# Kernel optimization log

Hardware: AMD Instinct MI355X
Metric: run time of the kernel (lower is better)

## Reference

```python
import jax, jax.numpy as jnp
import numpy as np

DIM = 1024
HEADS = 16
DIM_HEAD = 64
INNER = HEADS * DIM_HEAD
SCALE = DIM_HEAD ** -0.5


def rotate_half(t):
    # '... (j d) -> ... j d' with j=2: split last dim in half
    x1, x2 = jnp.split(t, 2, axis=-1)
    return jnp.concatenate((-x2, x1), axis=-1)


def rotary_pos(n, d, dtype):
    inv_freq = 1.0 / (10000.0 ** (jnp.arange(0, d, 2, dtype=jnp.float32) / d))
    freqs = jnp.arange(n, dtype=jnp.float32)[:, None] * inv_freq[None, :]  # (n, d/2)
    return jnp.concatenate((freqs, freqs), axis=-1).astype(dtype)  # (n, d)


def apply_rope(pos, t):
    return t * jnp.cos(pos) + rotate_half(t) * jnp.sin(pos)


def setup_inputs() -> dict:
    key = jax.random.key(0)
    ks = jax.random.split(key, 5)
    x = jax.random.normal(ks[0], (2, 2048, DIM), dtype=jnp.float32)
    gamma = jnp.ones((DIM,), dtype=jnp.float32)
    beta = jnp.zeros((DIM,), dtype=jnp.float32)
    Wq = jax.random.normal(ks[1], (DIM, INNER), dtype=jnp.float32) * 0.02
    Wkv = jax.random.normal(ks[2], (DIM, 2 * INNER), dtype=jnp.float32) * 0.02
    Wo = jax.random.normal(ks[3], (INNER, DIM), dtype=jnp.float32) * 0.02
    return {"x": x, "gamma": gamma, "beta": beta, "Wq": Wq, "Wkv": Wkv, "Wo": Wo}


def reference(x, gamma, beta, Wq, Wkv, Wo):
    b, n, _ = x.shape
    # LayerNorm with learned gamma, fixed-zero beta buffer
    mu = jnp.mean(x, axis=-1, keepdims=True)
    var = jnp.var(x, axis=-1, keepdims=True)
    xn = (x - mu) / jnp.sqrt(var + 1e-5) * gamma + beta

    q = xn @ Wq                       # (b, n, inner)
    kv = xn @ Wkv
    k, v = jnp.split(kv, 2, axis=-1)

    def to_heads(t):
        return t.reshape(b, n, HEADS, DIM_HEAD).transpose(0, 2, 1, 3)  # b h n d

    q, k, v = map(to_heads, (q, k, v))

    pos = rotary_pos(n, DIM_HEAD, x.dtype)  # (n, d)
    q = apply_rope(pos, q)
    k = apply_rope(pos, k)

    q = q * SCALE
    sim = jnp.einsum('bhid,bhjd->bhij', q, k)

    neg = -jnp.finfo(sim.dtype).max
    causal_mask = jnp.triu(jnp.ones((n, n), dtype=bool), k=1)
    sim = jnp.where(causal_mask, neg, sim)

    attn = jax.nn.softmax(sim, axis=-1)
    out = jnp.einsum('bhij,bhjd->bhid', attn, v)
    out = out.transpose(0, 2, 1, 3).reshape(b, n, INNER)
    return out @ Wo
```

## Files before the change

### kernel.cpp

```cpp
#include <hip/hip_runtime.h>
#include <stdint.h>

typedef unsigned short u16;
typedef __attribute__((ext_vector_type(8))) short short8;
typedef __attribute__((ext_vector_type(4))) float floatx4;
typedef __attribute__((ext_vector_type(4))) unsigned short u16x4;
typedef __attribute__((ext_vector_type(2))) unsigned int uint2v;

__device__ __forceinline__ float bf2f(u16 v) {
  union { uint32_t u; float f; } x; x.u = ((uint32_t)v) << 16; return x.f;
}
__device__ __forceinline__ u16 f2bf(float f) {
  union { float f; uint32_t u; } x; x.f = f;
  uint32_t r = x.u + 0x7fffu + ((x.u >> 16) & 1u);
  return (u16)(r >> 16);
}
__device__ __forceinline__ uint32_t fu(float f) {
  union { float f; uint32_t u; } x; x.f = f; return x.u;
}

#define GL2LDS(g, l)                                                          \
  __builtin_amdgcn_global_load_lds(                                           \
      (const __attribute__((address_space(1))) void*)(g),                     \
      (__attribute__((address_space(3))) void*)(l), 16, 0, 0)

__global__ __launch_bounds__(256) void prep_k(const float* __restrict__ x,
                                              const float* __restrict__ gamma,
                                              const float* __restrict__ beta,
                                              const float* __restrict__ Wq,
                                              const float* __restrict__ Wkv,
                                              const float* __restrict__ Wo,
                                              u16* __restrict__ xn,
                                              u16* __restrict__ wqkvT,
                                              u16* __restrict__ woT) {
  int bid = blockIdx.x;
  int t = threadIdx.x;
  if (bid < 4096) {
    int row = bid;
    const float* xr = x + (size_t)row * 1024;
    float4 xv = *(const float4*)(xr + t * 4);
    float v0 = xv.x, v1 = xv.y, v2 = xv.z, v3 = xv.w;
    float s = v0 + v1 + v2 + v3;
    float s2 = v0 * v0 + v1 * v1 + v2 * v2 + v3 * v3;
#pragma unroll
    for (int d = 1; d < 64; d <<= 1) {
      s += __shfl_xor(s, d, 64);
      s2 += __shfl_xor(s2, d, 64);
    }
    __shared__ float red[8];
    int lane = t & 63, wv = t >> 6;
    if (lane == 0) { red[wv] = s; red[4 + wv] = s2; }
    __syncthreads();
    s = red[0] + red[1] + red[2] + red[3];
    s2 = red[4] + red[5] + red[6] + red[7];
    float mu = s * (1.0f / 1024.0f);
    float var = s2 * (1.0f / 1024.0f) - mu * mu;
    float rstd = rsqrtf(var + 1e-5f);
    float4 gv = *(const float4*)(gamma + t * 4);
    float4 bv = *(const float4*)(beta + t * 4);
    u16x4 ov;
    ov.x = f2bf((v0 - mu) * rstd * gv.x + bv.x);
    ov.y = f2bf((v1 - mu) * rstd * gv.y + bv.y);
    ov.z = f2bf((v2 - mu) * rstd * gv.z + bv.z);
    ov.w = f2bf((v3 - mu) * rstd * gv.w + bv.w);
    *(u16x4*)(xn + (size_t)row * 1024 + t * 4) = ov;
  } else {
    __shared__ float tile[32][33];
    int wb = bid - 4096;
    const float* in;
    u16* outp;
    int C;
    if (wb < 1024) { in = Wq; outp = wqkvT; C = 1024; }
    else if (wb < 3072) { wb -= 1024; in = Wkv; outp = wqkvT + 1024 * 1024; C = 2048; }
    else { wb -= 3072; in = Wo; outp = woT; C = 1024; }
    int nbx = C >> 5;
    int c0 = (wb % nbx) * 32, r0 = (wb / nbx) * 32;
    int tx = t & 31, ty = t >> 5;
#pragma unroll
    for (int i = 0; i < 32; i += 8)
      tile[ty + i][tx] = in[(size_t)(r0 + ty + i) * C + c0 + tx];
    __syncthreads();
#pragma unroll
    for (int i = 0; i < 32; i += 8)
      outp[(size_t)(c0 + ty + i) * 1024 + r0 + tx] = f2bf(tile[tx][ty + i]);
  }
}

__global__ __launch_bounds__(256) void gemm_qkv_k(const u16* __restrict__ A,
                                                  const u16* __restrict__ BT,
                                                  u16* __restrict__ C) {
  const int K = 1024, lda = 1024, ldc = 3072;
  __shared__ __align__(16) u16 lA[128 * 32];
  __shared__ __align__(16) u16 lB[128 * 32];
  int tid = threadIdx.x;
  int bm = blockIdx.y * 128;
  int bn = blockIdx.x * 128;
  int w = tid >> 6, l = tid & 63;
  int wm = (w >> 1) * 64, wn = (w & 1) * 64;
  int lr = l & 15, lq = l >> 4;
  floatx4 acc[4][4] = {};
  int sr = w * 16 + (l >> 2);
  int sc = (l & 3) * 8;
  for (int k0 = 0; k0 < K; k0 += 32) {
    GL2LDS(A + (size_t)(bm + sr) * lda + k0 + sc, &lA[sr * 32 + sc]);
    GL2LDS(A + (size_t)(bm + sr + 64) * lda + k0 + sc, &lA[(sr + 64) * 32 + sc]);
    GL2LDS(BT + (size_t)(bn + sr) * K + k0 + sc, &lB[sr * 32 + sc]);
    GL2LDS(BT + (size_t)(bn + sr + 64) * K + k0 + sc, &lB[(sr + 64) * 32 + sc]);
    __syncthreads();
    short8 afr[4], bfr[4];
#pragma unroll
    for (int i = 0; i < 4; i++)
      afr[i] = *(const short8*)(&lA[(wm + i * 16 + lr) * 32 + lq * 8]);
#pragma unroll
    for (int i = 0; i < 4; i++)
      bfr[i] = *(const short8*)(&lB[(wn + i * 16 + lr) * 32 + lq * 8]);
#pragma unroll
    for (int mi = 0; mi < 4; mi++)
#pragma unroll
      for (int ni = 0; ni < 4; ni++)
        acc[mi][ni] = __builtin_amdgcn_mfma_f32_16x16x32_bf16(
            afr[mi], bfr[ni], acc[mi][ni], 0, 0, 0);
    __syncthreads();
  }
  int sec = bn >> 10;
  if (sec == 2) {
#pragma unroll
    for (int mi = 0; mi < 4; mi++)
#pragma unroll
      for (int ni = 0; ni < 4; ni++)
#pragma unroll
        for (int r = 0; r < 4; r++) {
          int row = bm + wm + mi * 16 + lq * 4 + r;
          int col = bn + wn + ni * 16 + lr;
          C[(size_t)row * ldc + col] = f2bf(acc[mi][ni][r]);
        }
  } else {
    float QS = (sec == 0) ? 0.125f * 1.44269504088896f : 1.0f;
#pragma unroll
    for (int ni = 0; ni < 2; ni++) {
      int i = ni * 16 + lr;
      float invf = exp2f(-(float)i * 0.4152410118609203f);
#pragma unroll
      for (int mi = 0; mi < 4; mi++)
#pragma unroll
        for (int r = 0; r < 4; r++) {
          int row = bm + wm + mi * 16 + lq * 4 + r;
          int n = row & 2047;
          float ang = (float)n * invf;
          float s_, c_;
          __sincosf(ang, &s_, &c_);
          float x1 = acc[mi][ni][r], x2 = acc[mi][ni + 2][r];
          int col = bn + wn + ni * 16 + lr;
          C[(size_t)row * ldc + col] = f2bf((x1 * c_ - x2 * s_) * QS);
          C[(size_t)row * ldc + col + 32] = f2bf((x2 * c_ + x1 * s_) * QS);
        }
    }
  }
}

__global__ __launch_bounds__(256) void gemm64_bf16_k(const u16* __restrict__ A,
                                                     const u16* __restrict__ BT,
                                                     float* __restrict__ C,
                                                     int K, int lda, int ldc) {
  __shared__ __align__(16) u16 lA[64 * 32];
  __shared__ __align__(16) u16 lB[128 * 32];
  int tid = threadIdx.x;
  int bm = blockIdx.y * 64;
  int bn = blockIdx.x * 128;
  int w = tid >> 6, l = tid & 63;
  int wm = (w >> 1) * 32, wn = (w & 1) * 64;
  int lr = l & 15, lq = l >> 4;
  floatx4 acc[2][4] = {};
  int sr = w * 16 + (l >> 2);
  int sc = (l & 3) * 8;
  for (int k0 = 0; k0 < K; k0 += 32) {
    GL2LDS(A + (size_t)(bm + sr) * lda + k0 + sc, &lA[sr * 32 + sc]);
    GL2LDS(BT + (size_t)(bn + sr) * K + k0 + sc, &lB[sr * 32 + sc]);
    GL2LDS(BT + (size_t)(bn + sr + 64) * K + k0 + sc, &lB[(sr + 64) * 32 + sc]);
    __syncthreads();
    short8 afr[2], bfr[4];
#pragma unroll
    for (int i = 0; i < 2; i++)
      afr[i] = *(const short8*)(&lA[(wm + i * 16 + lr) * 32 + lq * 8]);
#pragma unroll
    for (int i = 0; i < 4; i++)
      bfr[i] = *(const short8*)(&lB[(wn + i * 16 + lr) * 32 + lq * 8]);
#pragma unroll
    for (int mi = 0; mi < 2; mi++)
#pragma unroll
      for (int ni = 0; ni < 4; ni++)
        acc[mi][ni] = __builtin_amdgcn_mfma_f32_16x16x32_bf16(
            afr[mi], bfr[ni], acc[mi][ni], 0, 0, 0);
    __syncthreads();
  }
#pragma unroll
  for (int mi = 0; mi < 2; mi++)
#pragma unroll
    for (int ni = 0; ni < 4; ni++)
#pragma unroll
      for (int r = 0; r < 4; r++) {
        int row = bm + wm + mi * 16 + lq * 4 + r;
        int col = bn + wn + ni * 16 + lr;
        C[(size_t)row * ldc + col] = acc[mi][ni][r];
      }
}

__global__ __launch_bounds__(256) void vt_k(const u16* __restrict__ qkv,
                                            u16* __restrict__ vT) {
  __shared__ u16 tile[32][33];
  int vb = blockIdx.x;
  int bh = vb >> 7;
  int rest = vb & 127;
  int d0 = (rest >> 6) * 32;
  int n0 = (rest & 63) * 32;
  int b = bh >> 4, h = bh & 15;
  int tid = threadIdx.x;
  int tx = tid & 31, ty = tid >> 5;
#pragma unroll
  for (int i = 0; i < 32; i += 8)
    tile[ty + i][tx] =
        qkv[(size_t)(b * 2048 + n0 + ty + i) * 3072 + 2048 + h * 64 + d0 + tx];
  __syncthreads();
#pragma unroll
  for (int i = 0; i < 32; i += 8)
    vT[((size_t)bh * 64 + d0 + ty + i) * 2048 + n0 + tx] = tile[tx][ty + i];
}

#define LPT 72
#define FIXM 4.0f
__device__ __forceinline__ void attn_tile2(const u16* lK, const u16* lV, u16* lp,
                                           const short8* aq, floatx4* o,
                                           float& l_i, int lr, int lq,
                                           bool diag, int q0, int k0g,
                                           short8 ones) {
  floatx4 s[4];
#pragma unroll
  for (int ni = 0; ni < 4; ni++) {
    floatx4 a = {};
#pragma unroll
    for (int kc = 0; kc < 2; kc++) {
      int R = ni * 16 + lr;
      int c8 = (kc * 4 + lq) ^ (R & 7);
      short8 kf = *(const short8*)&lK[R * 64 + c8 * 8];
      a = __builtin_amdgcn_mfma_f32_16x16x32_bf16(kf, aq[kc], a, 0, 0, 0);
    }
    s[ni] = a;
  }
  if (diag) {
    int qg = q0 + lr;
#pragma unroll
    for (int ni = 0; ni < 4; ni++)
#pragma unroll
      for (int r = 0; r < 4; r++) {
        int kg = k0g + ni * 16 + lq * 4 + r;
        if (kg > qg) s[ni][r] = -1e30f;
      }
  }
#pragma unroll
  for (int ni = 0; ni < 4; ni++) {
    float p0 = exp2f(s[ni][0] - FIXM), p1 = exp2f(s[ni][1] - FIXM);
    float p2 = exp2f(s[ni][2] - FIXM), p3 = exp2f(s[ni][3] - FIXM);
    uint2v dw;
    dw.x = __builtin_amdgcn_perm(fu(p1), fu(p0), 0x07060302u);
    dw.y = __builtin_amdgcn_perm(fu(p3), fu(p2), 0x07060302u);
    *(uint2v*)&lp[lr * LPT + ni * 16 + lq * 4] = dw;
  }
  short8 pb0 = *(const short8*)&lp[lr * LPT + lq * 8];
  short8 pb1 = *(const short8*)&lp[lr * LPT + 32 + lq * 8];
  floatx4 z = {};
  z = __builtin_amdgcn_mfma_f32_16x16x32_bf16(ones, pb0, z, 0, 0, 0);
  z = __builtin_amdgcn_mfma_f32_16x16x32_bf16(ones, pb1, z, 0, 0, 0);
  l_i += z[0];
#pragma unroll
  for (int di = 0; di < 4; di++) {
    int R = di * 16 + lr;
    int c80 = lq ^ (R & 7);
    int c81 = (4 + lq) ^ (R & 7);
    short8 v0 = *(const short8*)&lV[R * 64 + c80 * 8];
    o[di] = __builtin_amdgcn_mfma_f32_16x16x32_bf16(v0, pb0, o[di], 0, 0, 0);
    short8 v1 = *(const short8*)&lV[R * 64 + c81 * 8];
    o[di] = __builtin_amdgcn_mfma_f32_16x16x32_bf16(v1, pb1, o[di], 0, 0, 0);
  }
}

__global__ __launch_bounds__(256) void attn_k(const u16* __restrict__ qkv,
                                              const u16* __restrict__ vt,
                                              u16* __restrict__ out) {
  __shared__ __align__(16) u16 lK[2][64 * 64];
  __shared__ __align__(16) u16 lV[2][64 * 64];
  __shared__ __align__(16) u16 lP[4][16 * LPT];
  int bh = blockIdx.y;
  int b = bh >> 4, h = bh & 15;
  int p = blockIdx.x;
  int jB = 31 - p;
  int tid = threadIdx.x;
  int w = tid >> 6, l = tid & 63;
  int lr = l & 15, lq = l >> 4;
  int q0A = p * 64 + w * 16;
  int q0B = jB * 64 + w * 16;
  const u16* qb = qkv + (size_t)b * 2048 * 3072 + h * 64;
  const u16* kb = qkv + (size_t)b * 2048 * 3072 + 1024 + h * 64;
  const u16* vb = vt + (size_t)bh * 64 * 2048;
  short8 aqA[2], aqB[2];
  aqA[0] = *(const short8*)(qb + (size_t)(q0A + lr) * 3072 + lq * 8);
  aqA[1] = *(const short8*)(qb + (size_t)(q0A + lr) * 3072 + 32 + lq * 8);
  aqB[0] = *(const short8*)(qb + (size_t)(q0B + lr) * 3072 + lq * 8);
  aqB[1] = *(const short8*)(qb + (size_t)(q0B + lr) * 3072 + 32 + lq * 8);
  short8 ones;
#pragma unroll
  for (int i = 0; i < 8; i++) ones[i] = (short)0x3F80;
  floatx4 oA[4] = {}, oB[4] = {};
  float lA_ = 0.0f, lB_ = 0.0f;
  int srow8 = l >> 3;
  int sc8 = (l & 7) ^ srow8;
  u16* lp = &lP[w][0];
  auto stage = [&](int bufi, int kt) {
#pragma unroll
    for (int c = 0; c < 2; c++) {
      int m = w + c * 4;
      int row = m * 8 + srow8;
      GL2LDS(kb + (size_t)(kt * 64 + row) * 3072 + sc8 * 8, &lK[bufi][m * 512]);
      GL2LDS(vb + (size_t)row * 2048 + kt * 64 + sc8 * 8, &lV[bufi][m * 512]);
    }
  };
  stage(0, 0);
  for (int kt = 0; kt <= jB; ++kt) {
    int cur = kt & 1;
    __syncthreads();
    if (kt < jB) stage(cur ^ 1, kt + 1);
    attn_tile2(lK[cur], lV[cur], lp, aqB, oB, lB_, lr, lq, kt == jB, q0B,
               kt * 64, ones);
    if (kt <= p)
      attn_tile2(lK[cur], lV[cur], lp, aqA, oA, lA_, lr, lq, kt == p, q0A,
                 kt * 64, ones);
  }
  float rlA = 1.0f / lA_, rlB = 1.0f / lB_;
#pragma unroll
  for (int di = 0; di < 4; di++) {
    uint2v dwA, dwB;
    u16 a0 = f2bf(oA[di][0] * rlA), a1 = f2bf(oA[di][1] * rlA);
    u16 a2 = f2bf(oA[di][2] * rlA), a3 = f2bf(oA[di][3] * rlA);
    dwA.x = (uint32_t)a0 | ((uint32_t)a1 << 16);
    dwA.y = (uint32_t)a2 | ((uint32_t)a3 << 16);
    u16 b0 = f2bf(oB[di][0] * rlB), b1 = f2bf(oB[di][1] * rlB);
    u16 b2 = f2bf(oB[di][2] * rlB), b3 = f2bf(oB[di][3] * rlB);
    dwB.x = (uint32_t)b0 | ((uint32_t)b1 << 16);
    dwB.y = (uint32_t)b2 | ((uint32_t)b3 << 16);
    int dcol = h * 64 + di * 16 + lq * 4;
    *(uint2v*)(out + ((size_t)(b * 2048 + q0A + lr)) * 3072 + dcol) = dwA;
    *(uint2v*)(out + ((size_t)(b * 2048 + q0B + lr)) * 3072 + dcol) = dwB;
  }
}

extern "C" void kernel_launch(void* const* d_in, const int* in_sizes, int n_in,
                              void* d_out, int out_size, void* d_ws, size_t ws_size,
                              hipStream_t stream) {
  const float* x = (const float*)d_in[0];
  const float* gamma = (const float*)d_in[1];
  const float* beta = (const float*)d_in[2];
  const float* Wq = (const float*)d_in[3];
  const float* Wkv = (const float*)d_in[4];
  const float* Wo = (const float*)d_in[5];
  float* out = (float*)d_out;
  char* ws = (char*)d_ws;

  u16* qkv = (u16*)(ws);
  u16* wqkvT = (u16*)(ws + 25165824);
  u16* woT = (u16*)(ws + 31457280);
  u16* xn = (u16*)(ws + 33554432);
  u16* vT = xn;
  u16* attn_out = qkv + 2048;

  prep_k<<<8192, 256, 0, stream>>>(x, gamma, beta, Wq, Wkv, Wo, xn, wqkvT, woT);
  gemm_qkv_k<<<dim3(24, 32), 256, 0, stream>>>(xn, wqkvT, qkv);
  vt_k<<<4096, 256, 0, stream>>>(qkv, vT);
  attn_k<<<dim3(16, 32), 256, 0, stream>>>(qkv, vT, attn_out);
  gemm64_bf16_k<<<dim3(8, 64), 256, 0, stream>>>(attn_out, woT, out, 1024, 3072, 1024);
}
```

Baseline: 208.9 us.

## Fuse V transpose into QKV GEMM epilogue and simplify attention block scheduling

The QKV GEMM epilogue now writes V already transposed (per batch-head, d-major) into the V section of the qkv buffer, which removes the separate vt_k transpose kernel and its extra global round trip. The attention kernel drops the paired-tile load balancing (pairing q-block p with 31-p) and launches one block per query tile, with batch-head on grid x. Attention output goes to a compact 1024-wide buffer. The per-warp P scratch drops its row padding and uses an XOR swizzle to avoid LDS bank conflicts. Risks are causal work imbalance across blocks and strided 8-byte transposed stores in the GEMM epilogue.

Result: faster. 202.6 us (-3.0%).

```diff
diff --git a/kernel.cpp b/kernel.cpp
--- a/kernel.cpp
+++ b/kernel.cpp
@@ -127,13 +127,22 @@
 #pragma unroll
     for (int mi = 0; mi < 4; mi++)
 #pragma unroll
-      for (int ni = 0; ni < 4; ni++)
-#pragma unroll
-        for (int r = 0; r < 4; r++) {
-          int row = bm + wm + mi * 16 + lq * 4 + r;
-          int col = bn + wn + ni * 16 + lr;
-          C[(size_t)row * ldc + col] = f2bf(acc[mi][ni][r]);
-        }
+      for (int ni = 0; ni < 4; ni++) {
+        int col = bn + wn + ni * 16 + lr;
+        int cv = col - 2048;
+        int row = bm + wm + mi * 16 + lq * 4;
+        int bq = row >> 11;
+        int n = row & 2047;
+        int bh = (bq << 4) | (cv >> 6);
+        int d = cv & 63;
+        size_t L = ((size_t)(bh * 64 + d) << 11) + n;
+        u16x4 ov;
+        ov.x = f2bf(acc[mi][ni][0]);
+        ov.y = f2bf(acc[mi][ni][1]);
+        ov.z = f2bf(acc[mi][ni][2]);
+        ov.w = f2bf(acc[mi][ni][3]);
+        *(u16x4*)(C + (L >> 10) * 3072 + 2048 + (L & 1023)) = ov;
+      }
   } else {
     float QS = (sec == 0) ? 0.125f * 1.44269504088896f : 1.0f;
 #pragma unroll
@@ -205,28 +214,7 @@
       }
 }
 
-__global__ __launch_bounds__(256) void vt_k(const u16* __restrict__ qkv,
-                                            u16* __restrict__ vT) {
-  __shared__ u16 tile[32][33];
-  int vb = blockIdx.x;
-  int bh = vb >> 7;
-  int rest = vb & 127;
-  int d0 = (rest >> 6) * 32;
-  int n0 = (rest & 63) * 32;
-  int b = bh >> 4, h = bh & 15;
-  int tid = threadIdx.x;
-  int tx = tid & 31, ty = tid >> 5;
-#pragma unroll
-  for (int i = 0; i < 32; i += 8)
-    tile[ty + i][tx] =
-        qkv[(size_t)(b * 2048 + n0 + ty + i) * 3072 + 2048 + h * 64 + d0 + tx];
-  __syncthreads();
-#pragma unroll
-  for (int i = 0; i < 32; i += 8)
-    vT[((size_t)bh * 64 + d0 + ty + i) * 2048 + n0 + tx] = tile[tx][ty + i];
-}
-
-#define LPT 72
+#define LPT 64
 #define FIXM 4.0f
 __device__ __forceinline__ void attn_tile2(const u16* lK, const u16* lV, u16* lp,
                                            const short8* aq, floatx4* o,
@@ -256,6 +244,7 @@
         if (kg > qg) s[ni][r] = -1e30f;
       }
   }
+  int swz = (lr & 7) << 3;
 #pragma unroll
   for (int ni = 0; ni < 4; ni++) {
     float p0 = exp2f(s[ni][0] - FIXM), p1 = exp2f(s[ni][1] - FIXM);
@@ -263,10 +252,10 @@
     uint2v dw;
     dw.x = __builtin_amdgcn_perm(fu(p1), fu(p0), 0x07060302u);
     dw.y = __builtin_amdgcn_perm(fu(p3), fu(p2), 0x07060302u);
-    *(uint2v*)&lp[lr * LPT + ni * 16 + lq * 4] = dw;
-  }
-  short8 pb0 = *(const short8*)&lp[lr * LPT + lq * 8];
-  short8 pb1 = *(const short8*)&lp[lr * LPT + 32 + lq * 8];
+    *(uint2v*)&lp[lr * LPT + ((ni * 16 + lq * 4) ^ swz)] = dw;
+  }
+  short8 pb0 = *(const short8*)&lp[lr * LPT + ((lq * 8) ^ swz)];
+  short8 pb1 = *(const short8*)&lp[lr * LPT + ((32 + lq * 8) ^ swz)];
   floatx4 z = {};
   z = __builtin_amdgcn_mfma_f32_16x16x32_bf16(ones, pb0, z, 0, 0, 0);
   z = __builtin_amdgcn_mfma_f32_16x16x32_bf16(ones, pb1, z, 0, 0, 0);
@@ -284,33 +273,28 @@
 }
 
 __global__ __launch_bounds__(256) void attn_k(const u16* __restrict__ qkv,
-                                              const u16* __restrict__ vt,
                                               u16* __restrict__ out) {
   __shared__ __align__(16) u16 lK[2][64 * 64];
   __shared__ __align__(16) u16 lV[2][64 * 64];
   __shared__ __align__(16) u16 lP[4][16 * LPT];
-  int bh = blockIdx.y;
+  int bh = blockIdx.x;
   int b = bh >> 4, h = bh & 15;
-  int p = blockIdx.x;
-  int jB = 31 - p;
+  int j = blockIdx.y;
   int tid = threadIdx.x;
   int w = tid >> 6, l = tid & 63;
   int lr = l & 15, lq = l >> 4;
-  int q0A = p * 64 + w * 16;
-  int q0B = jB * 64 + w * 16;
+  int q0 = j * 64 + w * 16;
   const u16* qb = qkv + (size_t)b * 2048 * 3072 + h * 64;
   const u16* kb = qkv + (size_t)b * 2048 * 3072 + 1024 + h * 64;
-  const u16* vb = vt + (size_t)bh * 64 * 2048;
-  short8 aqA[2], aqB[2];
-  aqA[0] = *(const short8*)(qb + (size_t)(q0A + lr) * 3072 + lq * 8);
-  aqA[1] = *(const short8*)(qb + (size_t)(q0A + lr) * 3072 + 32 + lq * 8);
-  aqB[0] = *(const short8*)(qb + (size_t)(q0B + lr) * 3072 + lq * 8);
-  aqB[1] = *(const short8*)(qb + (size_t)(q0B + lr) * 3072 + 32 + lq * 8);
+  int bh64 = bh * 64;
+  short8 aq[2];
+  aq[0] = *(const short8*)(qb + (size_t)(q0 + lr) * 3072 + lq * 8);
+  aq[1] = *(const short8*)(qb + (size_t)(q0 + lr) * 3072 + 32 + lq * 8);
   short8 ones;
 #pragma unroll
   for (int i = 0; i < 8; i++) ones[i] = (short)0x3F80;
-  floatx4 oA[4] = {}, oB[4] = {};
-  float lA_ = 0.0f, lB_ = 0.0f;
+  floatx4 o[4] = {};
+  float l_ = 0.0f;
   int srow8 = l >> 3;
   int sc8 = (l & 7) ^ srow8;
   u16* lp = &lP[w][0];
@@ -320,35 +304,30 @@
       int m = w + c * 4;
       int row = m * 8 + srow8;
       GL2LDS(kb + (size_t)(kt * 64 + row) * 3072 + sc8 * 8, &lK[bufi][m * 512]);
-      GL2LDS(vb + (size_t)row * 2048 + kt * 64 + sc8 * 8, &lV[bufi][m * 512]);
+      int nn = kt * 64 + sc8 * 8;
+      GL2LDS(qkv + (size_t)((bh64 + row) * 2 + (nn >> 10)) * 3072 + 2048 +
+                 (nn & 1023),
+             &lV[bufi][m * 512]);
     }
   };
   stage(0, 0);
-  for (int kt = 0; kt <= jB; ++kt) {
+  for (int kt = 0; kt <= j; ++kt) {
     int cur = kt & 1;
     __syncthreads();
-    if (kt < jB) stage(cur ^ 1, kt + 1);
-    attn_tile2(lK[cur], lV[cur], lp, aqB, oB, lB_, lr, lq, kt == jB, q0B,
-               kt * 64, ones);
-    if (kt <= p)
-      attn_tile2(lK[cur], lV[cur], lp, aqA, oA, lA_, lr, lq, kt == p, q0A,
-                 kt * 64, ones);
-  }
-  float rlA = 1.0f / lA_, rlB = 1.0f / lB_;
+    if (kt < j) stage(cur ^ 1, kt + 1);
+    attn_tile2(lK[cur], lV[cur], lp, aq, o, l_, lr, lq, kt == j, q0, kt * 64,
+               ones);
+  }
+  float rl = 1.0f / l_;
 #pragma unroll
   for (int di = 0; di < 4; di++) {
-    uint2v dwA, dwB;
-    u16 a0 = f2bf(oA[di][0] * rlA), a1 = f2bf(oA[di][1] * rlA);
-    u16 a2 = f2bf(oA[di][2] * rlA), a3 = f2bf(oA[di][3] * rlA);
-    dwA.x = (uint32_t)a0 | ((uint32_t)a1 << 16);
-    dwA.y = (uint32_t)a2 | ((uint32_t)a3 << 16);
-    u16 b0 = f2bf(oB[di][0] * rlB), b1 = f2bf(oB[di][1] * rlB);
-    u16 b2 = f2bf(oB[di][2] * rlB), b3 = f2bf(oB[di][3] * rlB);
-    dwB.x = (uint32_t)b0 | ((uint32_t)b1 << 16);
-    dwB.y = (uint32_t)b2 | ((uint32_t)b3 << 16);
+    uint2v dw;
+    u16 a0 = f2bf(o[di][0] * rl), a1 = f2bf(o[di][1] * rl);
+    u16 a2 = f2bf(o[di][2] * rl), a3 = f2bf(o[di][3] * rl);
+    dw.x = (uint32_t)a0 | ((uint32_t)a1 << 16);
+    dw.y = (uint32_t)a2 | ((uint32_t)a3 << 16);
     int dcol = h * 64 + di * 16 + lq * 4;
-    *(uint2v*)(out + ((size_t)(b * 2048 + q0A + lr)) * 3072 + dcol) = dwA;
-    *(uint2v*)(out + ((size_t)(b * 2048 + q0B + lr)) * 3072 + dcol) = dwB;
+    *(uint2v*)(out + ((size_t)(b * 2048 + q0 + lr)) * 1024 + dcol) = dw;
   }
 }
 
@@ -368,12 +347,10 @@
   u16* wqkvT = (u16*)(ws + 25165824);
   u16* woT = (u16*)(ws + 31457280);
   u16* xn = (u16*)(ws + 33554432);
-  u16* vT = xn;
-  u16* attn_out = qkv + 2048;
+  u16* attn_out = xn;
 
   prep_k<<<8192, 256, 0, stream>>>(x, gamma, beta, Wq, Wkv, Wo, xn, wqkvT, woT);
   gemm_qkv_k<<<dim3(24, 32), 256, 0, stream>>>(xn, wqkvT, qkv);
-  vt_k<<<4096, 256, 0, stream>>>(qkv, vT);
-  attn_k<<<dim3(16, 32), 256, 0, stream>>>(qkv, vT, attn_out);
-  gemm64_bf16_k<<<dim3(8, 64), 256, 0, stream>>>(attn_out, woT, out, 1024, 3072, 1024);
-}
+  attn_k<<<dim3(32, 32), 256, 0, stream>>>(qkv, attn_out);
+  gemm64_bf16_k<<<dim3(8, 64), 256, 0, stream>>>(attn_out, woT, out, 1024, 1024, 1024);
+}
```
